# Kernel tuning notes

Measured on AMD Instinct MI355X. Metric: run time of the kernel, lower is better.

## Reference

```python
import jax, jax.numpy as jnp
import numpy as np

B, N, C_S, C_Z, C, H, PQ, PV = 1, 512, 384, 128, 16, 12, 4, 8
N_BLOCKS = 8
SCALE, EPS, INF = 10.0, 1e-8, 1e5
N_RESTYPES = 5
CAT = H * C + 4 * H * PV + H * C_Z  # IPA output concat width = 2112


def layer_norm(x, g, b):
    mu = jnp.mean(x, -1, keepdims=True)
    var = jnp.mean(jnp.square(x - mu), -1, keepdims=True)
    return (x - mu) * jax.lax.rsqrt(var + 1e-5) * g + b


def quat_mul(q, p):
    w1, x1, y1, z1 = q[..., 0], q[..., 1], q[..., 2], q[..., 3]
    w2, x2, y2, z2 = p[..., 0], p[..., 1], p[..., 2], p[..., 3]
    return jnp.stack([
        w1 * w2 - x1 * x2 - y1 * y2 - z1 * z2,
        w1 * x2 + x1 * w2 + y1 * z2 - z1 * y2,
        w1 * y2 - x1 * z2 + y1 * w2 + z1 * x2,
        w1 * z2 + x1 * y2 - y1 * x2 + z1 * w2], -1)


def quat_to_rot(q):
    w, x, y, z = q[..., 0], q[..., 1], q[..., 2], q[..., 3]
    r0 = jnp.stack([w * w + x * x - y * y - z * z, 2 * (x * y - w * z), 2 * (x * z + w * y)], -1)
    r1 = jnp.stack([2 * (x * y + w * z), w * w - x * x + y * y - z * z, 2 * (y * z - w * x)], -1)
    r2 = jnp.stack([2 * (x * z - w * y), 2 * (y * z + w * x), w * w - x * x - y * y + z * z], -1)
    return jnp.stack([r0, r1, r2], -2)  # [..., 3, 3]


def _forward(single, pair, restype, mask,
             ln_s_g, ln_s_b, ln_z_g, ln_z_b, w_in, b_in,
             wq, bq, wkv, bkv, wqp, bqp, wkvp, bkvp, wb, bb_z, head_w, wo, bo,
             ln_ipa_g, ln_ipa_b, t_w1, t_b1, t_w2, t_b2, t_w3, t_b3, ln_t_g, ln_t_b,
             w_bb, b_bb, lit_pos):
    Bv, Nv = single.shape[0], single.shape[1]
    s = layer_norm(single, ln_s_g, ln_s_b)
    z = layer_norm(pair, ln_z_g, ln_z_b)
    s = s @ w_in + b_in
    quats = jnp.zeros((Bv, Nv, 4), s.dtype).at[..., 0].set(1.0)  # identity rigid, quat fmt
    trans = jnp.zeros((Bv, Nv, 3), s.dtype)
    mask_bias = INF * (mask[..., :, None] * mask[..., None, :] - 1.0)  # [B,N,N]
    hw = jax.nn.softplus(head_w) * np.float32(np.sqrt(1.0 / (3.0 * (PQ * 9.0 / 2.0))))
    zb = jnp.transpose(z @ wb + bb_z, (0, 3, 1, 2))  # [B,H,N,N] pair bias, same each block
    lit = lit_pos[restype]  # [B,N,3atoms,3] literature backbone coords

    def run_ipa(s, rot, tr):
        q = (s @ wq + bq).reshape(Bv, Nv, H, C)
        kv = (s @ wkv + bkv).reshape(Bv, Nv, H, 2 * C)
        k, v = kv[..., :C], kv[..., C:]
        qp = (s @ wqp + bqp).reshape(Bv, Nv, 3, H * PQ).swapaxes(-1, -2)
        qp = (jnp.einsum('bnij,bnpj->bnpi', rot, qp) + tr[..., None, :]).reshape(Bv, Nv, H, PQ, 3)
        kvp = (s @ wkvp + bkvp).reshape(Bv, Nv, 3, H * (PQ + PV)).swapaxes(-1, -2)
        kvp = (jnp.einsum('bnij,bnpj->bnpi', rot, kvp) + tr[..., None, :]).reshape(Bv, Nv, H, PQ + PV, 3)
        kp, vp = kvp[..., :PQ, :], kvp[..., PQ:, :]
        a = jnp.einsum('bihc,bjhc->bhij', q, k) * np.float32(np.sqrt(1.0 / (3 * C)))
        a = a + np.float32(np.sqrt(1.0 / 3.0)) * zb
        d2 = jnp.sum(jnp.square(qp[:, :, None] - kp[:, None]), -1)  # [B,N,N,H,PQ]
        pt_att = -0.5 * jnp.sum(d2 * hw[:, None], -1)  # [B,N,N,H]
        a = jax.nn.softmax(a + jnp.transpose(pt_att, (0, 3, 1, 2)) + mask_bias[:, None], -1)
        o = jnp.einsum('bhij,bjhc->bihc', a, v).reshape(Bv, Nv, H * C)
        opt = jnp.einsum('bhij,bjhpx->bihpx', a, vp)  # attended points, global frame
        opt = jnp.einsum('bnji,bnhpj->bnhpi', rot, opt - tr[:, :, None, None, :])  # invert_apply
        opt_norm = jnp.sqrt(jnp.sum(jnp.square(opt), -1) + EPS).reshape(Bv, Nv, H * PV)
        opt_flat = jnp.moveaxis(opt.reshape(Bv, Nv, H * PV, 3), -1, -2).reshape(Bv, Nv, 3 * H * PV)
        opair = jnp.einsum('bhij,bijc->bihc', a, z).reshape(Bv, Nv, H * C_Z)
        return jnp.concatenate([o, opt_flat, opt_norm, opair], -1) @ wo + bo

    frames_l, pos_l, states_l = [], [], []
    for _ in range(N_BLOCKS):
        rot = quat_to_rot(quats)
        s = s + run_ipa(s, rot, trans)
        s = layer_norm(s, ln_ipa_g, ln_ipa_b)  # ipa dropout = identity (eval)
        t = jax.nn.relu(s @ t_w1 + t_b1)
        t = jax.nn.relu(t @ t_w2 + t_b2)
        s = layer_norm(s + t @ t_w3 + t_b3, ln_t_g, ln_t_b)  # transition (1 layer) + LN
        upd = s @ w_bb + b_bb  # [B,N,6] backbone update
        pq = jnp.concatenate([jnp.ones_like(upd[..., :1]), upd[..., :3]], -1)
        nq = quat_mul(quats, pq)
        quats = nq * jax.lax.rsqrt(jnp.sum(jnp.square(nq), -1, keepdims=True))
        trans = trans + jnp.einsum('bnij,bnj->bni', rot, upd[..., 3:])  # OLD rot applies t-update
        rot_new = quat_to_rot(quats)
        pos_l.append(jnp.einsum('bnij,bnaj->bnai', rot_new, lit) + SCALE * trans[..., None, :])
        frames_l.append(jnp.concatenate([quats, SCALE * trans], -1))
        states_l.append(s)
        quats = jax.lax.stop_gradient(quats)  # stop_rot_gradient
    return jnp.stack(frames_l), jnp.stack(pos_l), jnp.stack(states_l), s


def setup_inputs() -> dict:
    key = jax.random.key(0)
    ki = iter(jax.random.split(key, 48))
    def w(fan_in, fan_out):
        return jax.random.normal(next(ki), (fan_in, fan_out), jnp.float32) / np.sqrt(fan_in)
    inp = {
        "single": jax.random.normal(next(ki), (B, N, C_S), jnp.float32),
        "pair": jax.random.normal(next(ki), (B, N, N, C_Z), jnp.float32),
        "restype": jax.random.randint(next(ki), (B, N), 0, N_RESTYPES),
        "mask": jnp.ones((B, N), jnp.float32),
        "ln_s_g": jnp.ones((C_S,)), "ln_s_b": jnp.zeros((C_S,)),
        "ln_z_g": jnp.ones((C_Z,)), "ln_z_b": jnp.zeros((C_Z,)),
        "w_in": w(C_S, C_S), "b_in": jnp.zeros((C_S,)),
        "wq": w(C_S, H * C), "bq": jnp.zeros((H * C,)),
        "wkv": w(C_S, 2 * H * C), "bkv": jnp.zeros((2 * H * C,)),
        "wqp": w(C_S, H * PQ * 3), "bqp": jnp.zeros((H * PQ * 3,)),
        "wkvp": w(C_S, H * (PQ + PV) * 3), "bkvp": jnp.zeros((H * (PQ + PV) * 3,)),
        "wb": w(C_Z, H), "bb_z": jnp.zeros((H,)),
        "head_w": 0.1 * jax.random.normal(next(ki), (H,), jnp.float32),
        "wo": w(CAT, C_S), "bo": jnp.zeros((C_S,)),
        "ln_ipa_g": jnp.ones((C_S,)), "ln_ipa_b": jnp.zeros((C_S,)),
        "t_w1": w(C_S, C_S), "t_b1": jnp.zeros((C_S,)),
        "t_w2": w(C_S, C_S), "t_b2": jnp.zeros((C_S,)),
        "t_w3": w(C_S, C_S), "t_b3": jnp.zeros((C_S,)),
        "ln_t_g": jnp.ones((C_S,)), "ln_t_b": jnp.zeros((C_S,)),
        "w_bb": 0.001 * jax.random.normal(next(ki), (C_S, 6), jnp.float32),
        "b_bb": jnp.zeros((6,)),
        "lit_pos": jax.random.normal(next(ki), (N_RESTYPES, 3, 3), jnp.float32),
    }
    return inp


def reference(single, pair, restype, mask,
              ln_s_g, ln_s_b, ln_z_g, ln_z_b, w_in, b_in,
              wq, bq, wkv, bkv, wqp, bqp, wkvp, bkvp, wb, bb_z, head_w, wo, bo,
              ln_ipa_g, ln_ipa_b, t_w1, t_b1, t_w2, t_b2, t_w3, t_b3, ln_t_g, ln_t_b,
              w_bb, b_bb, lit_pos):
    return _forward(single, pair, restype, mask,
                    ln_s_g, ln_s_b, ln_z_g, ln_z_b, w_in, b_in,
                    wq, bq, wkv, bkv, wqp, bqp, wkvp, bkvp, wb, bb_z, head_w, wo, bo,
                    ln_ipa_g, ln_ipa_b, t_w1, t_b1, t_w2, t_b2, t_w3, t_b3, ln_t_g, ln_t_b,
                    w_bb, b_bb, lit_pos)
```

## Files before the change

kernel.cpp:

```cpp
#include <hip/hip_runtime.h>
#include <hip/hip_bf16.h>
#include <math.h>

typedef __hip_bfloat16 bf16;

#define DINL __device__ __forceinline__
DINL float b2f(bf16 x){ return __bfloat162float(x); }
DINL bf16 f2b(float x){ return __float2bfloat16(x); }

DINL float ldin(const void* p, size_t i, int isb){
    return isb ? b2f(((const bf16*)p)[i]) : ((const float*)p)[i];
}
DINL void stout(void* p, size_t i, float v, int isb){
    if(isb) ((bf16*)p)[i] = f2b(v); else ((float*)p)[i] = v;
}

static constexpr int NRES = 512;
static constexpr int CS   = 384;
static constexpr int CZ   = 128;
static constexpr int NH   = 12;
static constexpr int PQn  = 4;
static constexpr int CAT  = 2112;
static constexpr int ASTR = 516;
static constexpr int ZSTR = 136;
static constexpr int SAK  = 56;
static constexpr int KSTR = 40;

typedef __attribute__((ext_vector_type(8))) short short8;
typedef __attribute__((ext_vector_type(4))) float f32x4;

__global__ void k_detect(const void* __restrict__ mask, int* __restrict__ flag){
    if(threadIdx.x==0 && blockIdx.x==0)
        flag[0] = (((const unsigned short*)mask)[0] == 0x3F80) ? 1 : 0;
}

#define MAXSEG 32
struct ConvSegs {
    const void* src[MAXSEG];
    int dst_off[MAXSEG];
    int blk0[MAXSEG];
    int total[MAXSEG];
};

__global__ void k_conv_multi(ConvSegs sg, int nseg, float* __restrict__ wsf,
                             const int* __restrict__ dt){
    int isb = dt[0];
    int b = blockIdx.x;
    int s = 0;
    #pragma unroll 1
    while(s+1 < nseg && sg.blk0[s+1] <= b) ++s;
    int idx = (b - sg.blk0[s])*256 + threadIdx.x;
    if(idx >= sg.total[s]) return;
    wsf[(size_t)sg.dst_off[s] + idx] = ldin(sg.src[s], idx, isb);
}

#define MAXTSEG 12
struct TSegs {
    const void* src[MAXTSEG];
    size_t dst_off[MAXTSEG];
    int N[MAXTSEG];
    int dstK[MAXTSEG];
    int blk0[MAXTSEG];
    int total[MAXTSEG];
};

__global__ void k_transpose_multi(TSegs sg, int nseg, bf16* __restrict__ base,
                                  const int* __restrict__ dt){
    int isb = dt[0];
    int b = blockIdx.x;
    int s = 0;
    #pragma unroll 1
    while(s+1 < nseg && sg.blk0[s+1] <= b) ++s;
    int idx = (b - sg.blk0[s])*256 + threadIdx.x;
    if(idx >= sg.total[s]) return;
    int N = sg.N[s];
    int k = idx / N, n = idx - k*N;
    base[sg.dst_off[s] + (size_t)n*sg.dstK[s] + k] = f2b(ldin(sg.src[s], idx, isb));
}

__global__ void k_wbT(const void* __restrict__ wb, bf16* __restrict__ wbT,
                      const int* __restrict__ dt){
    int isb = dt[0];
    for(int idx=threadIdx.x; idx<16*CZ; idx+=256){
        int nn = idx>>7, kk = idx&127;
        float v = (nn < NH) ? ldin(wb, (size_t)kk*NH+nn, isb) : 0.f;
        wbT[idx] = f2b(v);
    }
}

__global__ void k_init_frames(float* __restrict__ quats, float* __restrict__ trans){
    int i = blockIdx.x*blockDim.x + threadIdx.x;
    if(i < NRES){
        quats[i*4+0]=1.f; quats[i*4+1]=0.f; quats[i*4+2]=0.f; quats[i*4+3]=0.f;
        trans[i*3+0]=0.f; trans[i*3+1]=0.f; trans[i*3+2]=0.f;
    }
}

__global__ __launch_bounds__(128) void k_ln(const void* __restrict__ in, int in_dyn,
                     float* __restrict__ out, bf16* __restrict__ out16,
                     const float* __restrict__ g, const float* __restrict__ b, int Cdim,
                     void* __restrict__ outp, size_t st_ofs, size_t fin_ofs, int mode,
                     const int* __restrict__ dt, int nsum,
                     const float* __restrict__ sbias, const float* __restrict__ sres){
    int row = blockIdx.x, tid = threadIdx.x;
    int isb = dt[0];
    int isb_in = in_dyn ? isb : 0;
    float s=0.f, s2=0.f, vals[3];
    int r=0;
    for(int c=tid; c<Cdim; c+=128, ++r){
        size_t idx = (size_t)row*Cdim + c;
        float v;
        if(nsum > 0){
            const float* pf = (const float*)in;
            v = sbias[c] + sres[idx];
            for(int p=0;p<nsum;p++) v += pf[(size_t)p*NRES*Cdim + idx];
        } else {
            v = ldin(in, idx, isb_in);
        }
        vals[r]=v; s+=v; s2+=v*v;
    }
    __shared__ float red[128], red2[128];
    red[tid]=s; red2[tid]=s2; __syncthreads();
    for(int st=64; st>0; st>>=1){ if(tid<st){ red[tid]+=red[tid+st]; red2[tid]+=red2[tid+st]; } __syncthreads(); }
    float mu = red[0]/Cdim;
    float var = red2[0]/Cdim - mu*mu;
    float rs = rsqrtf(var + 1e-5f);
    r=0;
    for(int c=tid; c<Cdim; c+=128, ++r){
        float v = (vals[r]-mu)*rs*g[c] + b[c];
        size_t idx = (size_t)row*Cdim + c;
        if(out)   out[idx] = v;
        if(out16) out16[idx] = f2b(v);
        if(mode >= 1){
            stout(outp, st_ofs + idx, v, isb);
            if(mode == 2) stout(outp, fin_ofs + idx, v, isb);
        }
    }
}

__global__ __launch_bounds__(256) void k_gemm_bf(const bf16* __restrict__ A,
        const bf16* __restrict__ BT, float* __restrict__ Cf, bf16* __restrict__ C16,
        const float* __restrict__ bias, const float* __restrict__ res,
        int M, int Nn, int K, int relu, int lda){
    __shared__ bf16 As[64*SAK];
    __shared__ bf16 Bs[64*SAK];
    int tid = threadIdx.x;
    int bm = blockIdx.y*64, bn = blockIdx.x*64;
    int kofs = blockIdx.z*K;
    int wave = tid>>6, lane = tid&63;
    int quad = lane>>4, m16 = lane&15;
    int wm = (wave>>1)*32, wn = (wave&1)*32;
    int srow = wave*16 + (lane>>2);
    int scol = (lane&3)*8;
    const bf16* Ag = A  + (size_t)(bm + srow)*lda + kofs + scol;
    const bf16* Bg = BT + (size_t)(bn + srow)*lda + kofs + scol;
    int ldw = srow*SAK + scol;
    f32x4 acc[2][2] = {};
    short8 ra = *(const short8*)Ag;
    short8 rb = *(const short8*)Bg;
    int nsteps = K >> 5;
    const short* Asp = (const short*)As;
    const short* Bsp = (const short*)Bs;
    for(int s=0; s<nsteps; ++s){
        __syncthreads();
        *(short8*)(As + ldw) = ra;
        *(short8*)(Bs + ldw) = rb;
        __syncthreads();
        if(s+1 < nsteps){
            ra = *(const short8*)(Ag + (size_t)(s+1)*32);
            rb = *(const short8*)(Bg + (size_t)(s+1)*32);
        }
        short8 a0 = *(const short8*)&Asp[(wm +      m16)*SAK + quad*8];
        short8 a1 = *(const short8*)&Asp[(wm + 16 + m16)*SAK + quad*8];
        short8 b0 = *(const short8*)&Bsp[(wn +      m16)*SAK + quad*8];
        short8 b1 = *(const short8*)&Bsp[(wn + 16 + m16)*SAK + quad*8];
        acc[0][0] = __builtin_amdgcn_mfma_f32_16x16x32_bf16(a0, b0, acc[0][0], 0,0,0);
        acc[0][1] = __builtin_amdgcn_mfma_f32_16x16x32_bf16(a0, b1, acc[0][1], 0,0,0);
        acc[1][0] = __builtin_amdgcn_mfma_f32_16x16x32_bf16(a1, b0, acc[1][0], 0,0,0);
        acc[1][1] = __builtin_amdgcn_mfma_f32_16x16x32_bf16(a1, b1, acc[1][1], 0,0,0);
    }
    float* Cfz = Cf ? Cf + (size_t)blockIdx.z*M*Nn : nullptr;
    #pragma unroll
    for(int tm=0;tm<2;tm++){
        #pragma unroll
        for(int r=0;r<4;r++){
            int row = bm + wm + tm*16 + quad*4 + r;
            #pragma unroll
            for(int tn=0;tn<2;tn++){
                int col = bn + wn + tn*16 + m16;
                float v = acc[tm][tn][r];
                if(bias) v += bias[col];
                if(res)  v += res[(size_t)row*Nn + col];
                if(relu) v = fmaxf(v, 0.f);
                if(Cfz) Cfz[(size_t)row*Nn + col] = v;
                if(C16) C16[(size_t)row*Nn + col] = f2b(v);
            }
        }
    }
}

__global__ __launch_bounds__(256) void k_zb_mfma(const void* __restrict__ pair,
        const float* __restrict__ gz, const float* __restrict__ bz,
        const bf16* __restrict__ wbT, bf16* __restrict__ zb16,
        bf16* __restrict__ zn16, const int* __restrict__ dt){
    int isb = dt[0];
    __shared__ float gs[CZ], bs[CZ];
    int t = threadIdx.x;
    if(t < CZ){ gs[t]=gz[t]; bs[t]=bz[t]; }
    __syncthreads();
    int wave = t>>6, lane = t&63;
    int m = lane&15, quad = lane>>4;
    short8 bfrag[4];
    const short* wbs = (const short*)wbT;
    #pragma unroll
    for(int kc=0;kc<4;kc++) bfrag[kc] = *(const short8*)(wbs + m*CZ + kc*32 + quad*8);
    int rbase = blockIdx.x*256 + wave*64;
    for(int tile=0;tile<4;tile++){
        int row = rbase + tile*16 + m;
        float vals[32];
        #pragma unroll
        for(int kc=0;kc<4;kc++){
            int c0 = kc*32 + quad*8;
            size_t pb = (size_t)row*CZ + c0;
            if(isb){
                short8 pr = *(const short8*)((const short*)pair + pb);
                #pragma unroll
                for(int j=0;j<8;j++) vals[kc*8+j] = b2f(((const bf16*)&pr)[j]);
            } else {
                const float* pf = (const float*)pair + pb;
                #pragma unroll
                for(int j=0;j<8;j++) vals[kc*8+j] = pf[j];
            }
        }
        float s=0.f, s2=0.f;
        #pragma unroll
        for(int j=0;j<32;j++){ float v=vals[j]; s+=v; s2+=v*v; }
        s  += __shfl_xor(s,16,64);  s  += __shfl_xor(s,32,64);
        s2 += __shfl_xor(s2,16,64); s2 += __shfl_xor(s2,32,64);
        float mu = s*(1.f/CZ);
        float var = s2*(1.f/CZ) - mu*mu;
        float rsd = rsqrtf(var + 1e-5f);
        f32x4 acc = {0.f,0.f,0.f,0.f};
        #pragma unroll
        for(int kc=0;kc<4;kc++){
            int c0 = kc*32 + quad*8;
            short8 a;
            #pragma unroll
            for(int j=0;j<8;j++){
                float zn = (vals[kc*8+j]-mu)*rsd*gs[c0+j] + bs[c0+j];
                ((bf16*)&a)[j] = f2b(zn);
            }
            *(short8*)((short*)zn16 + (size_t)row*CZ + c0) = a;
            acc = __builtin_amdgcn_mfma_f32_16x16x32_bf16(a, bfrag[kc], acc, 0, 0, 0);
        }
        int col = lane&15;
        if(col < NH){
            unsigned short pk[4];
            #pragma unroll
            for(int r=0;r<4;r++){ bf16 h = f2b(acc[r]); pk[r] = *(unsigned short*)&h; }
            size_t o = (size_t)col*((size_t)NRES*NRES) + (size_t)(rbase + tile*16 + quad*4);
            *(uint2*)((unsigned short*)zb16 + o) = *(const uint2*)pk;
        }
    }
}


__global__ __launch_bounds__(192) void k_rotate_kv(const float* __restrict__ q_all,
        const float* __restrict__ quats, const float* __restrict__ trans,
        float* __restrict__ rot,
        float* __restrict__ qp_rot, float* __restrict__ kp_rot, bf16* __restrict__ vp16,
        float* __restrict__ k_buf, bf16* __restrict__ v16){
    int i = blockIdx.x, t = threadIdx.x;
    __shared__ float R[9], T[3];
    if(t==0){
        float w=quats[i*4],x=quats[i*4+1],y=quats[i*4+2],z=quats[i*4+3];
        R[0]=w*w+x*x-y*y-z*z; R[1]=2.f*(x*y-w*z);     R[2]=2.f*(x*z+w*y);
        R[3]=2.f*(x*y+w*z);   R[4]=w*w-x*x+y*y-z*z;   R[5]=2.f*(y*z-w*x);
        R[6]=2.f*(x*z-w*y);   R[7]=2.f*(y*z+w*x);     R[8]=w*w-x*x-y*y+z*z;
    }
    if(t<3) T[t] = trans[i*3+t];
    __syncthreads();
    if(t<9) rot[i*9+t] = R[t];
    const float* row = q_all + (size_t)i*1152;
    {
        int h = t/16, c = t%16;
        k_buf[((size_t)h*NRES + i)*16 + c] = row[192 + h*32 + c];
        v16[(size_t)i*192 + t]             = f2b(row[192 + h*32 + 16 + c]);
    }
    if(t < 48){
        float vx = row[576 + t], vy = row[576 + 48 + t], vz = row[576 + 96 + t];
        float* o = qp_rot + ((size_t)i*48 + t)*3;
        o[0] = R[0]*vx + R[1]*vy + R[2]*vz + T[0];
        o[1] = R[3]*vx + R[4]*vy + R[5]*vz + T[1];
        o[2] = R[6]*vx + R[7]*vy + R[8]*vz + T[2];
    }
    if(t < 144){
        int hp = t;
        float vx = row[720 + hp], vy = row[720 + 144 + hp], vz = row[720 + 288 + hp];
        float ox = R[0]*vx + R[1]*vy + R[2]*vz + T[0];
        float oy = R[3]*vx + R[4]*vy + R[5]*vz + T[1];
        float oz = R[6]*vx + R[7]*vy + R[8]*vz + T[2];
        int h = hp/12, p = hp%12;
        if(p < PQn){
            float* o = kp_rot + ((size_t)i*48 + h*4 + p)*3;
            o[0]=ox; o[1]=oy; o[2]=oz;
        } else {
            bf16* o = vp16 + ((size_t)i*96 + h*8 + (p-4))*3;
            o[0]=f2b(ox); o[1]=f2b(oy); o[2]=f2b(oz);
        }
    }
}

__global__ __launch_bounds__(256) void k_attn(const float* __restrict__ q_all,
        const float* __restrict__ k_buf, const float* __restrict__ qp_rot,
        const float* __restrict__ kp_rot, const bf16* __restrict__ zb16,
        const float* __restrict__ hw_f, const float* __restrict__ bbz_f,
        const void* __restrict__ mask, bf16* __restrict__ a16,
        const int* __restrict__ dt){
    int i0 = blockIdx.x*16, h = blockIdx.y;
    int t = threadIdx.x;
    int isb = dt[0];
    __shared__ bf16 kb_s[NRES*KSTR];
    __shared__ bf16 zb_s[16*NRES];
    __shared__ bf16 as_s[16*KSTR];
    __shared__ float colc_s[NRES];
    __shared__ float mcol_s[NRES];
    __shared__ float rowc_s[16], mrow_s[16];
    __shared__ float redm[4][16], reds[4][16];
    float hwx = hw_f[h];
    float sp = (hwx > 20.f) ? hwx : log1pf(expf(hwx));
    float hw = sp * 0.13608276348795434f;
    float zbb = 0.57735026919f * bbz_f[h];
    #pragma unroll
    for(int rr=0; rr<2; ++rr){
        int j = t*2 + rr;
        const float* kr  = k_buf  + ((size_t)h*NRES + j)*16;
        const float* kpr = kp_rot + ((size_t)j*48 + h*4)*3;
        bf16* dstp = kb_s + j*KSTR;
        #pragma unroll
        for(int c=0;c<16;c++) dstp[c] = f2b(kr[c]);
        float s2k = 0.f;
        #pragma unroll
        for(int p=0;p<12;p++){ float v = kpr[p]; s2k += v*v; dstp[16+p] = f2b(v); }
        dstp[28]=f2b(0.f); dstp[29]=f2b(0.f); dstp[30]=f2b(0.f); dstp[31]=f2b(0.f);
        colc_s[j] = -0.5f*hw*s2k;
        mcol_s[j] = ldin(mask, j, isb);
    }
    {
        const short8* zsrc = (const short8*)((const unsigned short*)zb16 + (size_t)h*NRES*NRES + (size_t)i0*NRES);
        short8* zdst = (short8*)zb_s;
        #pragma unroll
        for(int r=0;r<4;r++) zdst[t + r*256] = zsrc[t + r*256];
    }
    if(t < 16){
        int m = t;
        const float* qr = q_all + (size_t)(i0+m)*1152 + h*16;
        bf16* dstp = as_s + m*KSTR;
        #pragma unroll
        for(int c=0;c<16;c++) dstp[c] = f2b(qr[c]*0.14433756729740643f);
        const float* qpr = qp_rot + ((size_t)(i0+m)*48 + h*4)*3;
        float s2q = 0.f;
        #pragma unroll
        for(int p=0;p<12;p++){ float v = qpr[p]; s2q += v*v; dstp[16+p] = f2b(v*hw); }
        dstp[28]=f2b(0.f); dstp[29]=f2b(0.f); dstp[30]=f2b(0.f); dstp[31]=f2b(0.f);
        rowc_s[m] = -0.5f*hw*s2q;
        mrow_s[m] = ldin(mask, i0+m, isb);
    }
    __syncthreads();
    int lane = t&63, wv = t>>6;
    int quad = lane>>4, m16 = lane&15;
    short8 afrag = *(const short8*)((const short*)as_s + m16*KSTR + quad*8);
    float l[8][4];
    #pragma unroll
    for(int tt=0; tt<8; ++tt){
        int jt = wv*8 + tt;
        short8 bfrag = *(const short8*)((const short*)kb_s + (jt*16+m16)*KSTR + quad*8);
        f32x4 acc = {0.f,0.f,0.f,0.f};
        acc = __builtin_amdgcn_mfma_f32_16x16x32_bf16(afrag, bfrag, acc, 0,0,0);
        int j = jt*16 + m16;
        float cc = colc_s[j] + zbb;
        float mj = mcol_s[j];
        #pragma unroll
        for(int r=0;r<4;r++){
            int row = quad*4 + r;
            float zbv = b2f(zb_s[row*NRES + j]);
            l[tt][r] = acc[r] + 0.57735026919f*zbv + cc + rowc_s[row]
                     + 100000.0f*(mrow_s[row]*mj - 1.0f);
        }
    }
    float lm[4], ls[4];
    #pragma unroll
    for(int r=0;r<4;r++){
        float m = l[0][r];
        #pragma unroll
        for(int tt=1;tt<8;tt++) m = fmaxf(m, l[tt][r]);
        #pragma unroll
        for(int msk=1; msk<16; msk<<=1) m = fmaxf(m, __shfl_xor(m, msk, 64));
        lm[r] = m;
        float s = 0.f;
        #pragma unroll
        for(int tt=0;tt<8;tt++){ float e = expf(l[tt][r]-m); l[tt][r] = e; s += e; }
        #pragma unroll
        for(int msk=1; msk<16; msk<<=1) s += __shfl_xor(s, msk, 64);
        ls[r] = s;
    }
    if(m16 == 0){
        #pragma unroll
        for(int r=0;r<4;r++){ redm[wv][quad*4+r] = lm[r]; reds[wv][quad*4+r] = ls[r]; }
    }
    __syncthreads();
    #pragma unroll
    for(int r=0;r<4;r++){
        int row = quad*4+r;
        float M = redm[0][row];
        #pragma unroll
        for(int w=1;w<4;w++) M = fmaxf(M, redm[w][row]);
        float S = 0.f;
        #pragma unroll
        for(int w=0;w<4;w++) S += reds[w][row]*expf(redm[w][row]-M);
        float f = expf(lm[r]-M)/S;
        #pragma unroll
        for(int tt=0;tt<8;tt++){
            int j = (wv*8+tt)*16 + m16;
            a16[((size_t)h*NRES + i0+row)*NRES + j] = f2b(l[tt][r]*f);
        }
    }
}

__global__ __launch_bounds__(512) void k_attn_out(const bf16* __restrict__ a16,
        const bf16* __restrict__ v16, const bf16* __restrict__ vp16,
        const bf16* __restrict__ zn16,
        const float* __restrict__ rot, const float* __restrict__ trans,
        bf16* __restrict__ o_cat16){
    int i = blockIdx.x, t = threadIdx.x;
    __shared__ float a_sf[NH*ASTR];
    __shared__ bf16  zn_s[32*ZSTR];
    __shared__ float opt_s[288];
    for(int idx=t; idx<NH*NRES; idx+=512){
        int h = idx>>9, j = idx&511;
        a_sf[h*ASTR + j] = b2f(a16[((size_t)h*NRES + i)*NRES + j]);
    }
    int lane = t&63, quad = lane>>4, m16 = lane&15;
    int wv = t>>6;
    int jj = t>>4, c8 = (t&15)*8;
    int pc = t;
    int h0 = (pc<192) ? (pc>>4) : (pc-192)/24;
    const bf16* s0 = (pc<192) ? (v16 + pc) : (vp16 + (pc-192));
    int st0 = (pc<192) ? 192 : 288;
    const bf16* s1 = vp16 + 192 + t;
    int h1 = (192 + t)/24;
    float acc0 = 0.f, acc1 = 0.f;
    f32x4 macc[4] = {};
    __syncthreads();
    for(int j0=0; j0<NRES; j0+=32){
        if(j0) __syncthreads();
        {
            size_t pb = ((size_t)i*NRES + j0+jj)*CZ + c8;
            short8 z8 = *(const short8*)((const short*)zn16 + pb);
            *(short8*)&zn_s[jj*ZSTR + c8] = z8;
        }
        __syncthreads();
        if(wv < 6){
            const float* ap0 = a_sf + h0*ASTR;
            #pragma unroll
            for(int u=0; u<32; u+=4){
                int j = j0+u;
                float4 a4 = *(const float4*)(ap0 + j);
                acc0 += a4.x*b2f(s0[(size_t)j*st0])     + a4.y*b2f(s0[(size_t)(j+1)*st0])
                      + a4.z*b2f(s0[(size_t)(j+2)*st0]) + a4.w*b2f(s0[(size_t)(j+3)*st0]);
            }
            if(t < 96){
                const float* ap1 = a_sf + h1*ASTR;
                #pragma unroll
                for(int u=0; u<32; u+=4){
                    int j = j0+u;
                    float4 a4 = *(const float4*)(ap1 + j);
                    acc1 += a4.x*b2f(s1[(size_t)j*288])     + a4.y*b2f(s1[(size_t)(j+1)*288])
                          + a4.z*b2f(s1[(size_t)(j+2)*288]) + a4.w*b2f(s1[(size_t)(j+3)*288]);
                }
            }
        } else {
            float4 af0 = *(const float4*)&a_sf[m16*ASTR + j0 + quad*8];
            float4 af1 = *(const float4*)&a_sf[m16*ASTR + j0 + quad*8 + 4];
            short8 afrag;
            float az[8] = {af0.x,af0.y,af0.z,af0.w,af1.x,af1.y,af1.z,af1.w};
            #pragma unroll
            for(int r=0;r<8;r++) ((bf16*)&afrag)[r] = f2b((m16 < NH) ? az[r] : 0.f);
            int cbase = (wv-6)*64;
            #pragma unroll
            for(int tn=0; tn<4; ++tn){
                int c0 = cbase + tn*16;
                short8 bfrag;
                #pragma unroll
                for(int r=0;r<8;r++) ((bf16*)&bfrag)[r] = zn_s[(quad*8+r)*ZSTR + c0 + m16];
                macc[tn] = __builtin_amdgcn_mfma_f32_16x16x32_bf16(afrag, bfrag, macc[tn], 0,0,0);
            }
        }
    }
    if(wv >= 6){
        int cbase = (wv-6)*64;
        #pragma unroll
        for(int tn=0; tn<4; ++tn){
            int c = cbase + tn*16 + m16;
            #pragma unroll
            for(int r=0;r<4;r++){
                int h = quad*4 + r;
                if(h < NH) o_cat16[(size_t)i*CAT + 576 + h*CZ + c] = f2b(macc[tn][r]);
            }
        }
    } else {
        if(pc < 192) o_cat16[(size_t)i*CAT + pc] = f2b(acc0);
        else         opt_s[pc-192] = acc0;
        if(t < 96)   opt_s[192+t] = acc1;
    }
    __syncthreads();
    if(t < 96){
        float R0=rot[i*9+0],R1=rot[i*9+1],R2=rot[i*9+2];
        float R3=rot[i*9+3],R4=rot[i*9+4],R5=rot[i*9+5];
        float R6=rot[i*9+6],R7=rot[i*9+7],R8=rot[i*9+8];
        float T0=trans[i*3+0],T1=trans[i*3+1],T2=trans[i*3+2];
        const float* v = opt_s + t*3;
        float vx=v[0]-T0, vy=v[1]-T1, vz=v[2]-T2;
        float ox = R0*vx + R3*vy + R6*vz;
        float oy = R1*vx + R4*vy + R7*vz;
        float oz = R2*vx + R5*vy + R8*vz;
        bf16* o = o_cat16 + (size_t)i*CAT;
        o[192 +       t] = f2b(ox);
        o[192 +  96 + t] = f2b(oy);
        o[192 + 192 + t] = f2b(oz);
        o[480 + t] = f2b(sqrtf(ox*ox + oy*oy + oz*oz + 1e-8f));
    }
}

__global__ __launch_bounds__(64) void k_frames(const float* __restrict__ s,
        const float* __restrict__ wbb_f, const float* __restrict__ bbb_f,
        const float* __restrict__ rot, const int* __restrict__ restype,
        const float* __restrict__ lit_f,
        float* __restrict__ quats, float* __restrict__ trans,
        void* __restrict__ out, size_t frames_ofs, size_t pos_ofs,
        const int* __restrict__ dt){
    int i = blockIdx.x, lane = threadIdx.x;
    int isb = dt[0];
    const float* srow = s + (size_t)i*CS;
    float acc[6] = {};
    for(int k=lane; k<CS; k+=64){
        float sv = srow[k];
        #pragma unroll
        for(int j=0;j<6;j++) acc[j] += sv * wbb_f[k*6+j];
    }
    #pragma unroll
    for(int m=32; m>=1; m>>=1)
        #pragma unroll
        for(int j=0;j<6;j++) acc[j] += __shfl_xor(acc[j], m, 64);
    if(lane==0){
        float u[6];
        #pragma unroll
        for(int j=0;j<6;j++) u[j] = acc[j] + bbb_f[j];
        float qw=quats[i*4], qx=quats[i*4+1], qy=quats[i*4+2], qz=quats[i*4+3];
        float nw = qw       - qx*u[0] - qy*u[1] - qz*u[2];
        float nx = qw*u[0] + qx       + qy*u[2] - qz*u[1];
        float ny = qw*u[1] - qx*u[2] + qy       + qz*u[0];
        float nz = qw*u[2] + qx*u[1] - qy*u[0] + qz;
        float rn = rsqrtf(nw*nw + nx*nx + ny*ny + nz*nz);
        nw*=rn; nx*=rn; ny*=rn; nz*=rn;
        quats[i*4]=nw; quats[i*4+1]=nx; quats[i*4+2]=ny; quats[i*4+3]=nz;
        const float* R = rot + i*9;
        float tx = trans[i*3]   + R[0]*u[3]+R[1]*u[4]+R[2]*u[5];
        float ty = trans[i*3+1] + R[3]*u[3]+R[4]*u[4]+R[5]*u[5];
        float tz = trans[i*3+2] + R[6]*u[3]+R[7]*u[4]+R[8]*u[5];
        trans[i*3]=tx; trans[i*3+1]=ty; trans[i*3+2]=tz;
        size_t f = frames_ofs + (size_t)i*7;
        stout(out, f+0, nw, isb); stout(out, f+1, nx, isb);
        stout(out, f+2, ny, isb); stout(out, f+3, nz, isb);
        stout(out, f+4, 10.f*tx, isb); stout(out, f+5, 10.f*ty, isb); stout(out, f+6, 10.f*tz, isb);
        float Rn[9];
        Rn[0]=nw*nw+nx*nx-ny*ny-nz*nz; Rn[1]=2.f*(nx*ny-nw*nz);       Rn[2]=2.f*(nx*nz+nw*ny);
        Rn[3]=2.f*(nx*ny+nw*nz);       Rn[4]=nw*nw-nx*nx+ny*ny-nz*nz; Rn[5]=2.f*(ny*nz-nw*nx);
        Rn[6]=2.f*(nx*nz-nw*ny);       Rn[7]=2.f*(ny*nz+nw*nx);       Rn[8]=nw*nw-nx*nx-ny*ny+nz*nz;
        int rt = restype[i];
        size_t po = pos_ofs + (size_t)i*9;
        #pragma unroll
        for(int a=0;a<3;a++){
            float lx=lit_f[(rt*3+a)*3+0], ly=lit_f[(rt*3+a)*3+1], lz=lit_f[(rt*3+a)*3+2];
            stout(out, po+a*3+0, Rn[0]*lx + Rn[1]*ly + Rn[2]*lz + 10.f*tx, isb);
            stout(out, po+a*3+1, Rn[3]*lx + Rn[4]*ly + Rn[5]*lz + 10.f*ty, isb);
            stout(out, po+a*3+2, Rn[6]*lx + Rn[7]*ly + Rn[8]*lz + 10.f*tz, isb);
        }
    }
}


extern "C" void kernel_launch(void* const* d_in, const int* in_sizes, int n_in,
                              void* d_out, int out_size, void* d_ws, size_t ws_size,
                              hipStream_t stream){
    (void)in_sizes; (void)n_in; (void)out_size; (void)ws_size;
    const void* single = d_in[0];
    const void* pair   = d_in[1];
    const int*  restype= (const int*)d_in[2];
    const void* mask   = d_in[3];

    float* wsf = (float*)d_ws;
    bf16*  wsb = (bf16*)d_ws;
    size_t off = 0;
    auto alloc  = [&](size_t n){ float* p = wsf + off; off += (n + 3) & ~(size_t)3; return p; };
    auto allocB = [&](size_t n){ bf16* p = (bf16*)(wsf + off); off += ((n+1)/2 + 3) & ~(size_t)3; return p; };
    int*   dflag  = (int*)alloc(4);
    float* s      = alloc((size_t)NRES*CS);
    float* stmp   = alloc((size_t)NRES*CS);
    float* pw     = alloc((size_t)3*NRES*CS);
    float* q_all  = alloc((size_t)NRES*1152);
    float* qp_rot = alloc((size_t)NRES*144);
    float* kp_rot = alloc((size_t)NRES*144);
    float* k_bufp = alloc((size_t)NH*NRES*16);
    float* quats  = alloc(NRES*4);
    float* trans  = alloc(NRES*3);
    float* rot    = alloc(NRES*9);
    bf16*  a16    = allocB((size_t)NH*NRES*NRES);
    bf16*  zb16   = allocB((size_t)NH*NRES*NRES);
    bf16*  zn16   = allocB((size_t)NRES*NRES*CZ);
    bf16*  v16    = allocB((size_t)NRES*192);
    bf16*  vp16   = allocB((size_t)NRES*288);
    bf16*  o_cat16= allocB((size_t)NRES*CAT);
    bf16*  sin16  = allocB((size_t)NRES*CS);
    bf16*  s16    = allocB((size_t)NRES*CS);
    bf16*  t116   = allocB((size_t)NRES*CS);
    bf16*  t216   = allocB((size_t)NRES*CS);
    bf16*  WprojT = allocB((size_t)1152*CS);
    bf16*  w_inT  = allocB((size_t)CS*CS);
    bf16*  woT    = allocB((size_t)CS*CAT);
    bf16*  tw1T   = allocB((size_t)CS*CS);
    bf16*  tw2T   = allocB((size_t)CS*CS);
    bf16*  tw3T   = allocB((size_t)CS*CS);
    bf16*  wbT    = allocB(16*CZ);
    float* b_in_f = alloc(CS);
    float* bproj  = alloc(1152);
    float* bo_f   = alloc(CS);
    float* tb1f   = alloc(CS);
    float* tb2f   = alloc(CS);
    float* tb3f   = alloc(CS);
    float* lnsg   = alloc(CS);
    float* lnsb   = alloc(CS);
    float* lnig   = alloc(CS);
    float* lnib   = alloc(CS);
    float* lntg   = alloc(CS);
    float* lntb   = alloc(CS);
    float* gz_f   = alloc(CZ);
    float* bz_f   = alloc(CZ);
    float* bbz_f  = alloc(16);
    float* hw_f   = alloc(16);
    float* wbb_f  = alloc(CS*6);
    float* bbb_f  = alloc(8);
    float* lit_f  = alloc(48);

    const size_t OF_FRAMES = 0;
    const size_t OF_POS    = 28672;
    const size_t OF_STATES = 65536;
    const size_t OF_FINAL  = 1638400;

    auto cdiv = [](int a, int b){ return (a+b-1)/b; };

    k_detect<<<1,64,0,stream>>>(mask, dflag);

    ConvSegs sg;
    int nseg = 0, blk = 0;
    auto plain = [&](const void* src, float* dst, int total){
        sg.src[nseg]=src; sg.dst_off[nseg]=(int)(dst - wsf);
        sg.total[nseg]=total; sg.blk0[nseg]=blk;
        blk += (total+255)/256; ++nseg;
    };
    plain(d_in[11], bproj,     192);
    plain(d_in[13], bproj+192, 384);
    plain(d_in[15], bproj+576, 144);
    plain(d_in[17], bproj+720, 432);
    plain(d_in[9],  b_in_f, CS);
    plain(d_in[22], bo_f,   CS);
    plain(d_in[26], tb1f,   CS);
    plain(d_in[28], tb2f,   CS);
    plain(d_in[30], tb3f,   CS);
    plain(d_in[4],  lnsg,   CS);
    plain(d_in[5],  lnsb,   CS);
    plain(d_in[23], lnig,   CS);
    plain(d_in[24], lnib,   CS);
    plain(d_in[31], lntg,   CS);
    plain(d_in[32], lntb,   CS);
    plain(d_in[6],  gz_f,   CZ);
    plain(d_in[7],  bz_f,   CZ);
    plain(d_in[19], bbz_f,  NH);
    plain(d_in[20], hw_f,   NH);
    plain(d_in[34], bbb_f,  6);
    plain(d_in[35], lit_f,  45);
    plain(d_in[33], wbb_f,  CS*6);
    k_conv_multi<<<blk,256,0,stream>>>(sg, nseg, wsf, dflag);

    TSegs tg;
    int ntseg = 0, tblk = 0;
    auto trs = [&](const void* src, int K, int N, bf16* dst, int rowofs, int dstK){
        tg.src[ntseg]=src;
        tg.dst_off[ntseg]=(size_t)(dst - wsb) + (size_t)rowofs*dstK;
        tg.N[ntseg]=N; tg.dstK[ntseg]=dstK;
        tg.total[ntseg]=K*N; tg.blk0[ntseg]=tblk;
        tblk += (K*N+255)/256; ++ntseg;
    };
    trs(d_in[10], CS, 192, WprojT, 0,   CS);
    trs(d_in[12], CS, 384, WprojT, 192, CS);
    trs(d_in[14], CS, 144, WprojT, 576, CS);
    trs(d_in[16], CS, 432, WprojT, 720, CS);
    trs(d_in[8],  CS, CS,  w_inT,  0,   CS);
    trs(d_in[21], CAT, CS, woT,    0,   CAT);
    trs(d_in[25], CS, CS,  tw1T,   0,   CS);
    trs(d_in[27], CS, CS,  tw2T,   0,   CS);
    trs(d_in[29], CS, CS,  tw3T,   0,   CS);
    k_transpose_multi<<<tblk,256,0,stream>>>(tg, ntseg, wsb, dflag);
    k_wbT<<<1,256,0,stream>>>(d_in[18], wbT, dflag);

    k_zb_mfma<<<NRES*NRES/256,256,0,stream>>>(pair, gz_f, bz_f, wbT, zb16, zn16, dflag);

    k_ln<<<NRES,128,0,stream>>>(single, 1, nullptr, sin16, lnsg, lnsb, CS, nullptr, 0, 0, 0,
                                dflag, 0, nullptr, nullptr);
    {
        dim3 g(CS/64, NRES/64);
        k_gemm_bf<<<g,256,0,stream>>>(sin16, w_inT, s, s16, b_in_f, nullptr, NRES, CS, CS, 0, CS);
    }
    k_init_frames<<<cdiv(NRES,256),256,0,stream>>>(quats, trans);

    for(int bi=0; bi<8; ++bi){
        {
            dim3 g(1152/64, NRES/64);
            k_gemm_bf<<<g,256,0,stream>>>(s16, WprojT, q_all, nullptr, bproj, nullptr, NRES, 1152, CS, 0, CS);
        }
        k_rotate_kv<<<NRES,192,0,stream>>>(q_all, quats, trans, rot, qp_rot, kp_rot, vp16, k_bufp, v16);
        {
            dim3 g(NRES/16, NH);
            k_attn<<<g,256,0,stream>>>(q_all, k_bufp, qp_rot, kp_rot, zb16, hw_f, bbz_f, mask, a16, dflag);
        }
        k_attn_out<<<NRES,512,0,stream>>>(a16, v16, vp16, zn16, rot, trans, o_cat16);
        {
            dim3 gw(CS/64, NRES/64, 3);
            k_gemm_bf<<<gw,256,0,stream>>>(o_cat16, woT, pw, nullptr, nullptr, nullptr,
                                           NRES, CS, 704, 0, CAT);
            k_ln<<<NRES,128,0,stream>>>(pw, 0, s, s16, lnig, lnib, CS, nullptr, 0, 0, 0,
                                        dflag, 3, bo_f, s);
            dim3 g(CS/64, NRES/64);
            k_gemm_bf<<<g,256,0,stream>>>(s16,  tw1T, nullptr, t116, tb1f, nullptr, NRES, CS, CS, 1, CS);
            k_gemm_bf<<<g,256,0,stream>>>(t116, tw2T, nullptr, t216, tb2f, nullptr, NRES, CS, CS, 1, CS);
            k_gemm_bf<<<g,256,0,stream>>>(t216, tw3T, stmp, nullptr, tb3f, s, NRES, CS, CS, 0, CS);
            k_ln<<<NRES,128,0,stream>>>(stmp, 0, s, s16, lntg, lntb, CS, d_out,
                                        OF_STATES + (size_t)bi*NRES*CS, OF_FINAL,
                                        (bi==7) ? 2 : 1, dflag, 0, nullptr, nullptr);
        }
        k_frames<<<NRES,64,0,stream>>>(s, wbb_f, bbb_f, rot, restype, lit_f, quats, trans,
                                       d_out, OF_FRAMES + (size_t)bi*NRES*7,
                                       OF_POS + (size_t)bi*NRES*9, dflag);
    }
}
```

Before: 1.511 ms.

## Split-K projection GEMMs and fuse frame update into final layer norm

The QKV/point projection GEMM and the third transition GEMM now use a two-way split-K grid, which doubles the number of blocks. The partial sums are reduced, with bias added, in the kernels that consume them: k_rotate_kv sums the projection partials into shared memory, and the final layer norm sums the transition partials plus the residual. The separate k_frames kernel is removed and its backbone update is computed inside the last layer-norm kernel, saving one launch and a re-read of s per block. This costs extra partial-buffer traffic and a serial per-row frame computation on thread 0 of the layer-norm block.

```diff
diff --git a/kernel.cpp b/kernel.cpp
--- a/kernel.cpp
+++ b/kernel.cpp
@@ -101,7 +101,13 @@
                      const float* __restrict__ g, const float* __restrict__ b, int Cdim,
                      void* __restrict__ outp, size_t st_ofs, size_t fin_ofs, int mode,
                      const int* __restrict__ dt, int nsum,
-                     const float* __restrict__ sbias, const float* __restrict__ sres){
+                     const float* __restrict__ sbias, const float* __restrict__ sres,
+                     int do_frames,
+                     const float* __restrict__ wbb_f, const float* __restrict__ bbb_f,
+                     const float* __restrict__ rotp, const int* __restrict__ restype,
+                     const float* __restrict__ lit_f,
+                     float* __restrict__ quats, float* __restrict__ trans,
+                     size_t frames_ofs, size_t pos_ofs){
     int row = blockIdx.x, tid = threadIdx.x;
     int isb = dt[0];
     int isb_in = in_dyn ? isb : 0;
@@ -125,6 +131,7 @@
     float mu = red[0]/Cdim;
     float var = red2[0]/Cdim - mu*mu;
     float rs = rsqrtf(var + 1e-5f);
+    float facc[6] = {};
     r=0;
     for(int c=tid; c<Cdim; c+=128, ++r){
         float v = (vals[r]-mu)*rs*g[c] + b[c];
@@ -134,6 +141,59 @@
         if(mode >= 1){
             stout(outp, st_ofs + idx, v, isb);
             if(mode == 2) stout(outp, fin_ofs + idx, v, isb);
+        }
+        if(do_frames){
+            #pragma unroll
+            for(int j=0;j<6;j++) facc[j] += v * wbb_f[c*6+j];
+        }
+    }
+    if(do_frames){
+        int lane = tid&63, wv = tid>>6;
+        #pragma unroll
+        for(int m=32; m>=1; m>>=1)
+            #pragma unroll
+            for(int j=0;j<6;j++) facc[j] += __shfl_xor(facc[j], m, 64);
+        __shared__ float fred[2][6];
+        if(lane==0){
+            #pragma unroll
+            for(int j=0;j<6;j++) fred[wv][j] = facc[j];
+        }
+        __syncthreads();
+        if(tid==0){
+            int i = row;
+            float u[6];
+            #pragma unroll
+            for(int j=0;j<6;j++) u[j] = fred[0][j] + fred[1][j] + bbb_f[j];
+            float qw=quats[i*4], qx=quats[i*4+1], qy=quats[i*4+2], qz=quats[i*4+3];
+            float nw = qw       - qx*u[0] - qy*u[1] - qz*u[2];
+            float nx = qw*u[0] + qx       + qy*u[2] - qz*u[1];
+            float ny = qw*u[1] - qx*u[2] + qy       + qz*u[0];
+            float nz = qw*u[2] + qx*u[1] - qy*u[0] + qz;
+            float rn = rsqrtf(nw*nw + nx*nx + ny*ny + nz*nz);
+            nw*=rn; nx*=rn; ny*=rn; nz*=rn;
+            quats[i*4]=nw; quats[i*4+1]=nx; quats[i*4+2]=ny; quats[i*4+3]=nz;
+            const float* R = rotp + i*9;
+            float tx = trans[i*3]   + R[0]*u[3]+R[1]*u[4]+R[2]*u[5];
+            float ty = trans[i*3+1] + R[3]*u[3]+R[4]*u[4]+R[5]*u[5];
+            float tz = trans[i*3+2] + R[6]*u[3]+R[7]*u[4]+R[8]*u[5];
+            trans[i*3]=tx; trans[i*3+1]=ty; trans[i*3+2]=tz;
+            size_t f = frames_ofs + (size_t)i*7;
+            stout(outp, f+0, nw, isb); stout(outp, f+1, nx, isb);
+            stout(outp, f+2, ny, isb); stout(outp, f+3, nz, isb);
+            stout(outp, f+4, 10.f*tx, isb); stout(outp, f+5, 10.f*ty, isb); stout(outp, f+6, 10.f*tz, isb);
+            float Rn[9];
+            Rn[0]=nw*nw+nx*nx-ny*ny-nz*nz; Rn[1]=2.f*(nx*ny-nw*nz);       Rn[2]=2.f*(nx*nz+nw*ny);
+            Rn[3]=2.f*(nx*ny+nw*nz);       Rn[4]=nw*nw-nx*nx+ny*ny-nz*nz; Rn[5]=2.f*(ny*nz-nw*nx);
+            Rn[6]=2.f*(nx*nz-nw*ny);       Rn[7]=2.f*(ny*nz+nw*nx);       Rn[8]=nw*nw-nx*nx-ny*ny+nz*nz;
+            int rt = restype[i];
+            size_t po = pos_ofs + (size_t)i*9;
+            #pragma unroll
+            for(int a=0;a<3;a++){
+                float lx=lit_f[(rt*3+a)*3+0], ly=lit_f[(rt*3+a)*3+1], lz=lit_f[(rt*3+a)*3+2];
+                stout(outp, po+a*3+0, Rn[0]*lx + Rn[1]*ly + Rn[2]*lz + 10.f*tx, isb);
+                stout(outp, po+a*3+1, Rn[3]*lx + Rn[4]*ly + Rn[5]*lz + 10.f*ty, isb);
+                stout(outp, po+a*3+2, Rn[6]*lx + Rn[7]*ly + Rn[8]*lz + 10.f*tz, isb);
+            }
         }
     }
 }
@@ -265,13 +325,22 @@
 }
 
 
-__global__ __launch_bounds__(192) void k_rotate_kv(const float* __restrict__ q_all,
+__global__ __launch_bounds__(192) void k_rotate_kv(const float* __restrict__ qpw,
+        const float* __restrict__ bproj,
         const float* __restrict__ quats, const float* __restrict__ trans,
         float* __restrict__ rot,
         float* __restrict__ qp_rot, float* __restrict__ kp_rot, bf16* __restrict__ vp16,
-        float* __restrict__ k_buf, bf16* __restrict__ v16){
+        float* __restrict__ k_buf, bf16* __restrict__ v16, float* __restrict__ q_buf){
     int i = blockIdx.x, t = threadIdx.x;
     __shared__ float R[9], T[3];
+    __shared__ float rowbuf[1152];
+    const float* q0 = qpw + (size_t)i*1152;
+    const float* q1 = qpw + (size_t)NRES*1152 + (size_t)i*1152;
+    #pragma unroll
+    for(int r=0;r<6;r++){
+        int c = t + 192*r;
+        rowbuf[c] = q0[c] + q1[c] + bproj[c];
+    }
     if(t==0){
         float w=quats[i*4],x=quats[i*4+1],y=quats[i*4+2],z=quats[i*4+3];
         R[0]=w*w+x*x-y*y-z*z; R[1]=2.f*(x*y-w*z);     R[2]=2.f*(x*z+w*y);
@@ -281,14 +350,14 @@
     if(t<3) T[t] = trans[i*3+t];
     __syncthreads();
     if(t<9) rot[i*9+t] = R[t];
-    const float* row = q_all + (size_t)i*1152;
+    q_buf[(size_t)i*192 + t] = rowbuf[t];
     {
         int h = t/16, c = t%16;
-        k_buf[((size_t)h*NRES + i)*16 + c] = row[192 + h*32 + c];
-        v16[(size_t)i*192 + t]             = f2b(row[192 + h*32 + 16 + c]);
+        k_buf[((size_t)h*NRES + i)*16 + c] = rowbuf[192 + h*32 + c];
+        v16[(size_t)i*192 + t]             = f2b(rowbuf[192 + h*32 + 16 + c]);
     }
     if(t < 48){
-        float vx = row[576 + t], vy = row[576 + 48 + t], vz = row[576 + 96 + t];
+        float vx = rowbuf[576 + t], vy = rowbuf[576 + 48 + t], vz = rowbuf[576 + 96 + t];
         float* o = qp_rot + ((size_t)i*48 + t)*3;
         o[0] = R[0]*vx + R[1]*vy + R[2]*vz + T[0];
         o[1] = R[3]*vx + R[4]*vy + R[5]*vz + T[1];
@@ -296,7 +365,7 @@
     }
     if(t < 144){
         int hp = t;
-        float vx = row[720 + hp], vy = row[720 + 144 + hp], vz = row[720 + 288 + hp];
+        float vx = rowbuf[720 + hp], vy = rowbuf[720 + 144 + hp], vz = rowbuf[720 + 288 + hp];
         float ox = R[0]*vx + R[1]*vy + R[2]*vz + T[0];
         float oy = R[3]*vx + R[4]*vy + R[5]*vz + T[1];
         float oz = R[6]*vx + R[7]*vy + R[8]*vz + T[2];
@@ -311,7 +380,7 @@
     }
 }
 
-__global__ __launch_bounds__(256) void k_attn(const float* __restrict__ q_all,
+__global__ __launch_bounds__(256) void k_attn(const float* __restrict__ q_buf,
         const float* __restrict__ k_buf, const float* __restrict__ qp_rot,
         const float* __restrict__ kp_rot, const bf16* __restrict__ zb16,
         const float* __restrict__ hw_f, const float* __restrict__ bbz_f,
@@ -354,7 +423,7 @@
     }
     if(t < 16){
         int m = t;
-        const float* qr = q_all + (size_t)(i0+m)*1152 + h*16;
+        const float* qr = q_buf + (size_t)(i0+m)*192 + h*16;
         bf16* dstp = as_s + m*KSTR;
         #pragma unroll
         for(int c=0;c<16;c++) dstp[c] = f2b(qr[c]*0.14433756729740643f);
@@ -532,63 +601,6 @@
     }
 }
 
-__global__ __launch_bounds__(64) void k_frames(const float* __restrict__ s,
-        const float* __restrict__ wbb_f, const float* __restrict__ bbb_f,
-        const float* __restrict__ rot, const int* __restrict__ restype,
-        const float* __restrict__ lit_f,
-        float* __restrict__ quats, float* __restrict__ trans,
-        void* __restrict__ out, size_t frames_ofs, size_t pos_ofs,
-        const int* __restrict__ dt){
-    int i = blockIdx.x, lane = threadIdx.x;
-    int isb = dt[0];
-    const float* srow = s + (size_t)i*CS;
-    float acc[6] = {};
-    for(int k=lane; k<CS; k+=64){
-        float sv = srow[k];
-        #pragma unroll
-        for(int j=0;j<6;j++) acc[j] += sv * wbb_f[k*6+j];
-    }
-    #pragma unroll
-    for(int m=32; m>=1; m>>=1)
-        #pragma unroll
-        for(int j=0;j<6;j++) acc[j] += __shfl_xor(acc[j], m, 64);
-    if(lane==0){
-        float u[6];
-        #pragma unroll
-        for(int j=0;j<6;j++) u[j] = acc[j] + bbb_f[j];
-        float qw=quats[i*4], qx=quats[i*4+1], qy=quats[i*4+2], qz=quats[i*4+3];
-        float nw = qw       - qx*u[0] - qy*u[1] - qz*u[2];
-        float nx = qw*u[0] + qx       + qy*u[2] - qz*u[1];
-        float ny = qw*u[1] - qx*u[2] + qy       + qz*u[0];
-        float nz = qw*u[2] + qx*u[1] - qy*u[0] + qz;
-        float rn = rsqrtf(nw*nw + nx*nx + ny*ny + nz*nz);
-        nw*=rn; nx*=rn; ny*=rn; nz*=rn;
-        quats[i*4]=nw; quats[i*4+1]=nx; quats[i*4+2]=ny; quats[i*4+3]=nz;
-        const float* R = rot + i*9;
-        float tx = trans[i*3]   + R[0]*u[3]+R[1]*u[4]+R[2]*u[5];
-        float ty = trans[i*3+1] + R[3]*u[3]+R[4]*u[4]+R[5]*u[5];
-        float tz = trans[i*3+2] + R[6]*u[3]+R[7]*u[4]+R[8]*u[5];
-        trans[i*3]=tx; trans[i*3+1]=ty; trans[i*3+2]=tz;
-        size_t f = frames_ofs + (size_t)i*7;
-        stout(out, f+0, nw, isb); stout(out, f+1, nx, isb);
-        stout(out, f+2, ny, isb); stout(out, f+3, nz, isb);
-        stout(out, f+4, 10.f*tx, isb); stout(out, f+5, 10.f*ty, isb); stout(out, f+6, 10.f*tz, isb);
-        float Rn[9];
-        Rn[0]=nw*nw+nx*nx-ny*ny-nz*nz; Rn[1]=2.f*(nx*ny-nw*nz);       Rn[2]=2.f*(nx*nz+nw*ny);
-        Rn[3]=2.f*(nx*ny+nw*nz);       Rn[4]=nw*nw-nx*nx+ny*ny-nz*nz; Rn[5]=2.f*(ny*nz-nw*nx);
-        Rn[6]=2.f*(nx*nz-nw*ny);       Rn[7]=2.f*(ny*nz+nw*nx);       Rn[8]=nw*nw-nx*nx-ny*ny+nz*nz;
-        int rt = restype[i];
-        size_t po = pos_ofs + (size_t)i*9;
-        #pragma unroll
-        for(int a=0;a<3;a++){
-            float lx=lit_f[(rt*3+a)*3+0], ly=lit_f[(rt*3+a)*3+1], lz=lit_f[(rt*3+a)*3+2];
-            stout(out, po+a*3+0, Rn[0]*lx + Rn[1]*ly + Rn[2]*lz + 10.f*tx, isb);
-            stout(out, po+a*3+1, Rn[3]*lx + Rn[4]*ly + Rn[5]*lz + 10.f*ty, isb);
-            stout(out, po+a*3+2, Rn[6]*lx + Rn[7]*ly + Rn[8]*lz + 10.f*tz, isb);
-        }
-    }
-}
-
 
 extern "C" void kernel_launch(void* const* d_in, const int* in_sizes, int n_in,
                               void* d_out, int out_size, void* d_ws, size_t ws_size,
@@ -608,7 +620,8 @@
     float* s      = alloc((size_t)NRES*CS);
     float* stmp   = alloc((size_t)NRES*CS);
     float* pw     = alloc((size_t)3*NRES*CS);
-    float* q_all  = alloc((size_t)NRES*1152);
+    float* qpw    = alloc((size_t)2*NRES*1152);
+    float* q_buf  = alloc((size_t)NRES*192);
     float* qp_rot = alloc((size_t)NRES*144);
     float* kp_rot = alloc((size_t)NRES*144);
     float* k_bufp = alloc((size_t)NH*NRES*16);
@@ -716,7 +729,9 @@
     k_zb_mfma<<<NRES*NRES/256,256,0,stream>>>(pair, gz_f, bz_f, wbT, zb16, zn16, dflag);
 
     k_ln<<<NRES,128,0,stream>>>(single, 1, nullptr, sin16, lnsg, lnsb, CS, nullptr, 0, 0, 0,
-                                dflag, 0, nullptr, nullptr);
+                                dflag, 0, nullptr, nullptr,
+                                0, nullptr, nullptr, nullptr, nullptr, nullptr,
+                                nullptr, nullptr, 0, 0);
     {
         dim3 g(CS/64, NRES/64);
         k_gemm_bf<<<g,256,0,stream>>>(sin16, w_inT, s, s16, b_in_f, nullptr, NRES, CS, CS, 0, CS);
@@ -725,13 +740,15 @@
 
     for(int bi=0; bi<8; ++bi){
         {
-            dim3 g(1152/64, NRES/64);
-            k_gemm_bf<<<g,256,0,stream>>>(s16, WprojT, q_all, nullptr, bproj, nullptr, NRES, 1152, CS, 0, CS);
-        }
-        k_rotate_kv<<<NRES,192,0,stream>>>(q_all, quats, trans, rot, qp_rot, kp_rot, vp16, k_bufp, v16);
+            dim3 gp(1152/64, NRES/64, 2);
+            k_gemm_bf<<<gp,256,0,stream>>>(s16, WprojT, qpw, nullptr, nullptr, nullptr,
+                                           NRES, 1152, 192, 0, CS);
+        }
+        k_rotate_kv<<<NRES,192,0,stream>>>(qpw, bproj, quats, trans, rot, qp_rot, kp_rot,
+                                           vp16, k_bufp, v16, q_buf);
         {
             dim3 g(NRES/16, NH);
-            k_attn<<<g,256,0,stream>>>(q_all, k_bufp, qp_rot, kp_rot, zb16, hw_f, bbz_f, mask, a16, dflag);
+            k_attn<<<g,256,0,stream>>>(q_buf, k_bufp, qp_rot, kp_rot, zb16, hw_f, bbz_f, mask, a16, dflag);
         }
         k_attn_out<<<NRES,512,0,stream>>>(a16, v16, vp16, zn16, rot, trans, o_cat16);
         {
@@ -739,17 +756,22 @@
             k_gemm_bf<<<gw,256,0,stream>>>(o_cat16, woT, pw, nullptr, nullptr, nullptr,
                                            NRES, CS, 704, 0, CAT);
             k_ln<<<NRES,128,0,stream>>>(pw, 0, s, s16, lnig, lnib, CS, nullptr, 0, 0, 0,
-                                        dflag, 3, bo_f, s);
+                                        dflag, 3, bo_f, s,
+                                        0, nullptr, nullptr, nullptr, nullptr, nullptr,
+                                        nullptr, nullptr, 0, 0);
             dim3 g(CS/64, NRES/64);
             k_gemm_bf<<<g,256,0,stream>>>(s16,  tw1T, nullptr, t116, tb1f, nullptr, NRES, CS, CS, 1, CS);
             k_gemm_bf<<<g,256,0,stream>>>(t116, tw2T, nullptr, t216, tb2f, nullptr, NRES, CS, CS, 1, CS);
-            k_gemm_bf<<<g,256,0,stream>>>(t216, tw3T, stmp, nullptr, tb3f, s, NRES, CS, CS, 0, CS);
-            k_ln<<<NRES,128,0,stream>>>(stmp, 0, s, s16, lntg, lntb, CS, d_out,
+            dim3 g3(CS/64, NRES/64, 2);
+            k_gemm_bf<<<g3,256,0,stream>>>(t216, tw3T, pw, nullptr, nullptr, nullptr,
+                                           NRES, CS, 192, 0, CS);
+            k_ln<<<NRES,128,0,stream>>>(pw, 0, s, s16, lntg, lntb, CS, d_out,
                                         OF_STATES + (size_t)bi*NRES*CS, OF_FINAL,
-                                        (bi==7) ? 2 : 1, dflag, 0, nullptr, nullptr);
-        }
-        k_frames<<<NRES,64,0,stream>>>(s, wbb_f, bbb_f, rot, restype, lit_f, quats, trans,
-                                       d_out, OF_FRAMES + (size_t)bi*NRES*7,
-                                       OF_POS + (size_t)bi*NRES*9, dflag);
-    }
-}
+                                        (bi==7) ? 2 : 1, dflag, 2, tb3f, s,
+                                        1, wbb_f, bbb_f, rot, restype, lit_f,
+                                        quats, trans,
+                                        OF_FRAMES + (size_t)bi*NRES*7,
+                                        OF_POS + (size_t)bi*NRES*9);
+        }
+    }
+}
```

Measured after the change: 1.395 ms. 1.08x faster.
